# Optimization experiments

Hardware: AMD Instinct MI355X
Metric: run time of the kernel (lower is better)

Reference implementation:

```python
import jax, jax.numpy as jnp
import numpy as np

C_IN = 512
NUM_HEADS = 8
D_K = 64
D_V = 64


def setup_inputs() -> dict:
    key = jax.random.key(0)
    ks = jax.random.split(key, 6)
    scale = 1.0 / np.sqrt(C_IN)
    return {
        "x": jax.random.normal(ks[0], (8, C_IN, 32, 32), dtype=jnp.float32),
        "Wq": jax.random.normal(ks[1], (C_IN, NUM_HEADS * D_K), dtype=jnp.float32) * scale,
        "bq": jnp.zeros((NUM_HEADS * D_K,), dtype=jnp.float32),
        "Wk": jax.random.normal(ks[2], (C_IN, NUM_HEADS * D_K), dtype=jnp.float32) * scale,
        "bk": jnp.zeros((NUM_HEADS * D_K,), dtype=jnp.float32),
        "Wv": jax.random.normal(ks[3], (C_IN, NUM_HEADS * D_V), dtype=jnp.float32) * scale,
        "bv": jnp.zeros((NUM_HEADS * D_V,), dtype=jnp.float32),
        "Wo": jax.random.normal(ks[4], (NUM_HEADS * D_V, C_IN), dtype=jnp.float32) * scale,
        "bo": jnp.zeros((C_IN,), dtype=jnp.float32),
        "num_heads": NUM_HEADS,
    }


def reference(x, Wq, bq, Wk, bk, Wv, bv, Wo, bo, num_heads):
    B, C, H, W = x.shape
    S = H * W
    xs = x.reshape(B, C, S).transpose(0, 2, 1)  # [B, S, C]

    def split_heads(t):  # [B, S, nh*d] -> [B, nh, S, d]
        return t.reshape(B, S, num_heads, -1).transpose(0, 2, 1, 3)

    q = split_heads(xs @ Wq + bq)  # [B, nh, S, d_k]
    k = split_heads(xs @ Wk + bk)  # [B, nh, S, d_k]
    v = split_heads(xs @ Wv + bv)  # [B, nh, S, d_v]

    d_k = q.shape[-1]
    scores = jnp.einsum("bhqd,bhkd->bhqk", q, k) / jnp.sqrt(jnp.float32(d_k))
    probs = jax.nn.softmax(scores, axis=-1)
    attn = jnp.einsum("bhqk,bhkd->bhqd", probs, v)  # [B, nh, S, d_v]

    out = attn.transpose(0, 2, 1, 3).reshape(B, S, -1)  # [B, S, nh*d_v]
    out = out @ Wo + bo  # [B, S, C]
    out = out + xs  # residual
    return out.transpose(0, 2, 1).reshape(B, C, H, W)
```

## Files before the change

kernel.cpp:

```cpp
#include <hip/hip_runtime.h>

#define S_LEN 1024
#define CIN 512
#define NH 8
#define DH 64
#define NB 8

typedef short bf16x8 __attribute__((ext_vector_type(8)));
typedef float f32x4 __attribute__((ext_vector_type(4)));
typedef unsigned short u16x4 __attribute__((ext_vector_type(4)));

__device__ inline unsigned short f2bf(float f){
  union { float f; unsigned u; } v; v.f = f;
  unsigned r = v.u + 0x7FFFu + ((v.u >> 16) & 1u);
  return (unsigned short)(r >> 16);
}

__device__ inline unsigned cvt_pk_bf16(float a, float b){
  unsigned r;
  asm("v_cvt_pk_bf16_f32 %0, %1, %2" : "=v"(r) : "v"(a), "v"(b));
  return r;
}

__device__ inline void gload16(const void* g, void* l){
  __builtin_amdgcn_global_load_lds(
      (const __attribute__((address_space(1))) unsigned*)g,
      (__attribute__((address_space(3))) unsigned*)l, 16, 0, 0);
}

__device__ inline bf16x8 ldfrag(const unsigned short* lds, int row, int kbyte){
  return *(const bf16x8*)((const char*)lds + row*128 + (kbyte ^ ((row & 7) << 4)));
}

__global__ __launch_bounds__(256) void prep(const float* __restrict__ x,
    const float* __restrict__ Wq, const float* __restrict__ Wk,
    const float* __restrict__ Wv, const float* __restrict__ Wo,
    unsigned short* __restrict__ xs, unsigned short* __restrict__ Wqkt,
    unsigned short* __restrict__ Wvt, unsigned short* __restrict__ Wot){
  __shared__ unsigned short T[64*72];
  int bid = blockIdx.x, t = threadIdx.x;
  const float* src; unsigned short* dst; int ldS, r0, c0;
  if (bid < 1024){
    int b = bid >> 7, tt = bid & 127;
    src = x + (size_t)b*CIN*S_LEN; ldS = S_LEN;
    dst = xs + (size_t)b*S_LEN*CIN;
    r0 = (tt >> 4) * 64;
    c0 = (tt & 15) * 64;
  } else {
    int w = bid - 1024, mat = w >> 6, tt = w & 63;
    r0 = (tt >> 3) * 64; c0 = (tt & 7) * 64; ldS = 512;
    if (mat == 0){ src = Wq; dst = Wqkt; }
    else if (mat == 1){ src = Wk; dst = Wqkt + 512*512; }
    else if (mat == 2){ src = Wv; dst = Wvt; }
    else            { src = Wo; dst = Wot; }
  }
  int rl = t >> 4, cb = (t & 15) * 4;
  #pragma unroll
  for (int rr = 0; rr < 4; rr++){
    float4 f = *(const float4*)(src + (size_t)(r0 + rl + rr*16)*ldS + c0 + cb);
    int rc = rl + rr*16;
    T[(cb+0)*72 + rc] = f2bf(f.x);
    T[(cb+1)*72 + rc] = f2bf(f.y);
    T[(cb+2)*72 + rc] = f2bf(f.z);
    T[(cb+3)*72 + rc] = f2bf(f.w);
  }
  __syncthreads();
  int cl = t >> 2, rb = (t & 3) * 16;
  uint4 v0 = *(const uint4*)&T[cl*72 + rb];
  uint4 v1 = *(const uint4*)&T[cl*72 + rb + 8];
  *(uint4*)(dst + (size_t)(c0 + cl)*512 + r0 + rb) = v0;
  *(uint4*)(dst + (size_t)(c0 + cl)*512 + r0 + rb + 8) = v1;
}

__device__ inline void gemm128(const unsigned short* A, const unsigned short* B,
    unsigned short* As, unsigned short* Bs, f32x4 acc[4][4], int tid){
  int lane = tid & 63, w = tid >> 6;
  int wr = w >> 1, wc = w & 1;
  int srow = lane >> 3;
  int scol8 = ((lane & 7) ^ (lane >> 3)) << 3;
  for (int k0 = 0; k0 < 512; k0 += 64){
    __syncthreads();
    #pragma unroll
    for (int i = 0; i < 4; i++){
      int r0 = w*32 + i*8;
      gload16(A + (size_t)(r0 + srow)*512 + k0 + scol8, As + r0*64);
      gload16(B + (size_t)(r0 + srow)*512 + k0 + scol8, Bs + r0*64);
    }
    __syncthreads();
    #pragma unroll
    for (int kt = 0; kt < 2; kt++){
      bf16x8 af[4], bfv[4];
      #pragma unroll
      for (int i = 0; i < 4; i++){
        af[i]  = ldfrag(As, wr*64 + i*16 + (lane & 15), kt*64 + ((lane >> 4) << 4));
        bfv[i] = ldfrag(Bs, wc*64 + i*16 + (lane & 15), kt*64 + ((lane >> 4) << 4));
      }
      #pragma unroll
      for (int mi = 0; mi < 4; mi++)
        #pragma unroll
        for (int ni = 0; ni < 4; ni++)
          acc[mi][ni] = __builtin_amdgcn_mfma_f32_16x16x32_bf16(af[mi], bfv[ni], acc[mi][ni], 0,0,0);
    }
  }
}

__global__ __launch_bounds__(256) void qkv128(const unsigned short* __restrict__ xs,
    const unsigned short* __restrict__ Wqkt, const unsigned short* __restrict__ Wvt,
    const float* __restrict__ bq, const float* __restrict__ bk,
    const float* __restrict__ bv, unsigned short* __restrict__ q_ws,
    unsigned short* __restrict__ k_ws, unsigned short* __restrict__ vt_ws){
  __shared__ __align__(16) unsigned short As[8192], Bs[8192];
  int tid = threadIdx.x, lane = tid & 63, w = tid >> 6, wr = w >> 1, wc = w & 1;
  int bx = blockIdx.x, by = blockIdx.y, b = blockIdx.z;
  f32x4 acc[4][4];
  #pragma unroll
  for (int i = 0; i < 4; i++)
    #pragma unroll
    for (int j = 0; j < 4; j++) acc[i][j] = (f32x4){0.f,0.f,0.f,0.f};
  if (by < 8){
    int m0 = bx * 128, n0 = by * 128;
    gemm128(xs + (size_t)b*S_LEN*CIN + (size_t)m0*512, Wqkt + (size_t)n0*512, As, Bs, acc, tid);
    int jb = (n0 + wc*64) >> 6;
    int isK = jb >= 8, h = jb & 7;
    const float* bias = isK ? bk : bq;
    unsigned short* dst = (isK ? k_ws : q_ws) + ((size_t)(b*NH + h))*S_LEN*DH;
    #pragma unroll
    for (int nt = 0; nt < 4; nt++){
      int d = nt*16 + (lane & 15);
      float bb = bias[(jb & 7)*64 + d];
      #pragma unroll
      for (int mi = 0; mi < 4; mi++)
        #pragma unroll
        for (int r = 0; r < 4; r++){
          int s = m0 + wr*64 + mi*16 + (lane >> 4)*4 + r;
          dst[(size_t)s*DH + d] = f2bf(acc[mi][nt][r] + bb);
        }
    }
  } else {
    int m0 = (by - 8) * 128, n0 = bx * 128;
    gemm128(Wvt + (size_t)m0*512, xs + (size_t)b*S_LEN*CIN + (size_t)n0*512, As, Bs, acc, tid);
    #pragma unroll
    for (int mi = 0; mi < 4; mi++)
      #pragma unroll
      for (int r = 0; r < 4; r++){
        int j = m0 + wr*64 + mi*16 + (lane >> 4)*4 + r;
        int h = j >> 6, dv = j & 63;
        float bb = bv[j];
        unsigned short* dst = vt_ws + ((size_t)(b*NH + h)*DH + dv)*S_LEN;
        #pragma unroll
        for (int nt = 0; nt < 4; nt++){
          int s = n0 + wc*64 + nt*16 + (lane & 15);
          dst[s] = f2bf(acc[mi][nt][r] + bb);
        }
      }
  }
}

__global__ __launch_bounds__(512) void attn_fwd(const unsigned short* __restrict__ qw,
    const unsigned short* __restrict__ kw, const unsigned short* __restrict__ vtw,
    unsigned short* __restrict__ aw){
  __shared__ __align__(16) unsigned short Ks[2][4096], Vs[2][4096], Ps[8192];
  int tid = threadIdx.x, lane = tid & 63, wid = tid >> 6;
  int bid = blockIdx.x;
  int idx = bid >> 3;
  int qb = idx & 7;
  int bh = (bid & 7)*8 + (idx >> 3);
  int qrw = lane & 15, g = lane >> 4;
  int q0 = qb*128 + wid*16;
  const unsigned short* qrow = qw + ((size_t)bh*S_LEN + q0 + qrw)*DH;
  bf16x8 qf0 = *(const bf16x8*)(qrow + g*8);
  bf16x8 qf1 = *(const bf16x8*)(qrow + 32 + g*8);
  unsigned short* myP = Ps + wid*1024;
  f32x4 oacc[4];
  #pragma unroll
  for (int i = 0; i < 4; i++) oacc[i] = (f32x4){0.f,0.f,0.f,0.f};
  float mrun = -3e38f, lrun = 0.f;
  int srow = lane >> 3, scol8 = ((lane & 7) ^ (lane >> 3)) << 3;
  const unsigned short* kbase = kw + (size_t)bh*S_LEN*DH;
  const unsigned short* vbase = vtw + (size_t)bh*DH*S_LEN;
  const float SC = 0.125f * 1.44269504f;
  int r0 = wid*8;
  gload16(kbase + (size_t)(r0 + srow)*DH + scol8, Ks[0] + r0*64);
  gload16(vbase + (size_t)(r0 + srow)*S_LEN + scol8, Vs[0] + r0*64);
  __syncthreads();
  int cur = 0;

  for (int kv0 = 0; kv0 < S_LEN; kv0 += 64){
    if (kv0 + 64 < S_LEN){
      gload16(kbase + (size_t)(kv0 + 64 + r0 + srow)*DH + scol8, Ks[cur^1] + r0*64);
      gload16(vbase + (size_t)(r0 + srow)*S_LEN + kv0 + 64 + scol8, Vs[cur^1] + r0*64);
    }
    const unsigned short* Kc = Ks[cur];
    const unsigned short* Vc = Vs[cur];

    f32x4 st[4];
    #pragma unroll
    for (int mt = 0; mt < 4; mt++){
      f32x4 a = (f32x4){0.f,0.f,0.f,0.f};
      a = __builtin_amdgcn_mfma_f32_16x16x32_bf16(
            ldfrag(Kc, mt*16 + qrw, g << 4), qf0, a, 0,0,0);
      a = __builtin_amdgcn_mfma_f32_16x16x32_bf16(
            ldfrag(Kc, mt*16 + qrw, 64 + (g << 4)), qf1, a, 0,0,0);
      st[mt] = a;
    }
    float vmax = -3e38f;
    #pragma unroll
    for (int mt = 0; mt < 4; mt++)
      #pragma unroll
      for (int r = 0; r < 4; r++){
        st[mt][r] *= SC;
        vmax = fmaxf(vmax, st[mt][r]);
      }
    vmax = fmaxf(vmax, __shfl_xor(vmax, 16));
    vmax = fmaxf(vmax, __shfl_xor(vmax, 32));
    float mnew = fmaxf(mrun, vmax);
    float corr = __builtin_amdgcn_exp2f(mrun - mnew);
    float psum = 0.f;
    #pragma unroll
    for (int mt = 0; mt < 4; mt++){
      float p0 = __builtin_amdgcn_exp2f(st[mt][0] - mnew);
      float p1 = __builtin_amdgcn_exp2f(st[mt][1] - mnew);
      float p2 = __builtin_amdgcn_exp2f(st[mt][2] - mnew);
      float p3 = __builtin_amdgcn_exp2f(st[mt][3] - mnew);
      psum += (p0 + p1) + (p2 + p3);
      uint2 pw; pw.x = cvt_pk_bf16(p0, p1); pw.y = cvt_pk_bf16(p2, p3);
      *(uint2*)((char*)myP + qrw*128 + ((mt*32 + g*8) ^ ((qrw & 7) << 4))) = pw;
    }
    psum += __shfl_xor(psum, 16);
    psum += __shfl_xor(psum, 32);
    lrun = lrun * corr + psum;
    mrun = mnew;
    #pragma unroll
    for (int mt = 0; mt < 4; mt++) oacc[mt] *= corr;
    #pragma unroll
    for (int kt = 0; kt < 2; kt++){
      bf16x8 pf = *(const bf16x8*)((char*)myP + qrw*128 +
                    ((kt*64 + (g << 4)) ^ ((qrw & 7) << 4)));
      #pragma unroll
      for (int mt = 0; mt < 4; mt++)
        oacc[mt] = __builtin_amdgcn_mfma_f32_16x16x32_bf16(
            ldfrag(Vc, mt*16 + qrw, kt*64 + (g << 4)), pf, oacc[mt], 0,0,0);
    }
    __syncthreads();
    cur ^= 1;
  }
  float inv = 1.f / lrun;
  #pragma unroll
  for (int mt = 0; mt < 4; mt++){
    uint2 pw;
    pw.x = cvt_pk_bf16(oacc[mt][0] * inv, oacc[mt][1] * inv);
    pw.y = cvt_pk_bf16(oacc[mt][2] * inv, oacc[mt][3] * inv);
    *(uint2*)((char*)myP + qrw*128 + ((mt*32 + g*8) ^ ((qrw & 7) << 4))) = pw;
  }
  int b = bh >> 3, h = bh & 7;
  int rr = lane >> 2, cc = lane & 3;
  uint4 lo = *(const uint4*)((char*)myP + rr*128 + ((cc*32) ^ ((rr & 7) << 4)));
  uint4 hi = *(const uint4*)((char*)myP + rr*128 + (((cc*32) + 16) ^ ((rr & 7) << 4)));
  unsigned short* obase = aw + ((size_t)b*S_LEN + (q0 + rr))*512 + h*64 + cc*16;
  *(uint4*)obase = lo;
  *(uint4*)(obase + 8) = hi;
}

__global__ __launch_bounds__(256) void out128(const unsigned short* __restrict__ Wot,
    const unsigned short* __restrict__ aw, const float* __restrict__ bo,
    const float* __restrict__ x, float* __restrict__ out){
  __shared__ __align__(16) unsigned short As[8192], Bs[8192];
  int tid = threadIdx.x, lane = tid & 63, w = tid >> 6, wr = w >> 1, wc = w & 1;
  int m0 = blockIdx.x * 128, n0 = blockIdx.y * 128, b = blockIdx.z;
  f32x4 acc[4][4];
  #pragma unroll
  for (int i = 0; i < 4; i++)
    #pragma unroll
    for (int j = 0; j < 4; j++) acc[i][j] = (f32x4){0.f,0.f,0.f,0.f};
  gemm128(Wot + (size_t)m0*512, aw + (size_t)b*S_LEN*512 + (size_t)n0*512, As, Bs, acc, tid);
  #pragma unroll
  for (int mi = 0; mi < 4; mi++)
    #pragma unroll
    for (int r = 0; r < 4; r++){
      int c = m0 + wr*64 + mi*16 + (lane >> 4)*4 + r;
      float bb = bo[c];
      size_t rowb = ((size_t)b*CIN + c)*S_LEN;
      #pragma unroll
      for (int nt = 0; nt < 4; nt++){
        int s = n0 + wc*64 + nt*16 + (lane & 15);
        out[rowb + s] = acc[mi][nt][r] + bb + x[rowb + s];
      }
    }
}

extern "C" void kernel_launch(void* const* d_in, const int* in_sizes, int n_in,
                              void* d_out, int out_size, void* d_ws, size_t ws_size,
                              hipStream_t stream){
  const float* x  = (const float*)d_in[0];
  const float* Wq = (const float*)d_in[1];
  const float* bq = (const float*)d_in[2];
  const float* Wk = (const float*)d_in[3];
  const float* bk = (const float*)d_in[4];
  const float* Wv = (const float*)d_in[5];
  const float* bv = (const float*)d_in[6];
  const float* Wo = (const float*)d_in[7];
  const float* bo = (const float*)d_in[8];
  float* out = (float*)d_out;

  unsigned short* p = (unsigned short*)d_ws;
  const size_t xs_e   = (size_t)NB*S_LEN*CIN;
  const size_t qkv_e  = (size_t)NB*NH*S_LEN*DH;
  unsigned short* xs    = p;                 p += xs_e;
  unsigned short* Wqkt  = p;                 p += 1024*512;
  unsigned short* Wvt   = p;                 p += 512*512;
  unsigned short* Wot   = p;                 p += 512*512;
  unsigned short* q_ws  = p;                 p += qkv_e;
  unsigned short* k_ws  = p;                 p += qkv_e;
  unsigned short* vt_ws = p;                 p += qkv_e;
  unsigned short* aw    = p;                 p += qkv_e;

  prep<<<1280, 256, 0, stream>>>(x, Wq, Wk, Wv, Wo, xs, Wqkt, Wvt, Wot);
  qkv128<<<dim3(8, 12, NB), 256, 0, stream>>>(xs, Wqkt, Wvt, bq, bk, bv, q_ws, k_ws, vt_ws);
  attn_fwd<<<512, 512, 0, stream>>>(q_ws, k_ws, vt_ws, aw);
  out128<<<dim3(4, 8, NB), 256, 0, stream>>>(Wot, aw, bo, x, out);
}
```

Before: 156.5 us.

## Add lazy softmax rescaling, MFMA priority hints, and a 128x64 output GEMM tile

The attention loop now rescales the running max and accumulators only when some row's new max exceeds the old one by more than a threshold. This skips most per-tile exp and multiply work on the rescale path. The MFMA sections are wrapped in s_setprio to favour matrix issue across waves. The output projection uses a new 128x64 tile kernel with twice as many blocks to improve CU occupancy, at the cost of more global reloads of the weight tile. The lazy rescale lets probabilities exceed 1 by a bounded factor, which risks precision loss in bf16.

Result: faster. 151.8 us (-3.0%).

```diff
diff --git a/kernel.cpp b/kernel.cpp
--- a/kernel.cpp
+++ b/kernel.cpp
@@ -8,7 +8,7 @@
 
 typedef short bf16x8 __attribute__((ext_vector_type(8)));
 typedef float f32x4 __attribute__((ext_vector_type(4)));
-typedef unsigned short u16x4 __attribute__((ext_vector_type(4)));
+typedef float f32x2 __attribute__((ext_vector_type(2)));
 
 __device__ inline unsigned short f2bf(float f){
   union { float f; unsigned u; } v; v.f = f;
@@ -194,6 +194,7 @@
     const unsigned short* Vc = Vs[cur];
 
     f32x4 st[4];
+    __builtin_amdgcn_s_setprio(1);
     #pragma unroll
     for (int mt = 0; mt < 4; mt++){
       f32x4 a = (f32x4){0.f,0.f,0.f,0.f};
@@ -203,6 +204,7 @@
             ldfrag(Kc, mt*16 + qrw, 64 + (g << 4)), qf1, a, 0,0,0);
       st[mt] = a;
     }
+    __builtin_amdgcn_s_setprio(0);
     float vmax = -3e38f;
     #pragma unroll
     for (int mt = 0; mt < 4; mt++)
@@ -213,25 +215,29 @@
       }
     vmax = fmaxf(vmax, __shfl_xor(vmax, 16));
     vmax = fmaxf(vmax, __shfl_xor(vmax, 32));
-    float mnew = fmaxf(mrun, vmax);
-    float corr = __builtin_amdgcn_exp2f(mrun - mnew);
+    if (!__all(vmax <= mrun + 8.f)){
+      float mnew = fmaxf(mrun, vmax);
+      float corr = __builtin_amdgcn_exp2f(mrun - mnew);
+      lrun *= corr;
+      #pragma unroll
+      for (int mt = 0; mt < 4; mt++) oacc[mt] *= corr;
+      mrun = mnew;
+    }
     float psum = 0.f;
     #pragma unroll
     for (int mt = 0; mt < 4; mt++){
-      float p0 = __builtin_amdgcn_exp2f(st[mt][0] - mnew);
-      float p1 = __builtin_amdgcn_exp2f(st[mt][1] - mnew);
-      float p2 = __builtin_amdgcn_exp2f(st[mt][2] - mnew);
-      float p3 = __builtin_amdgcn_exp2f(st[mt][3] - mnew);
+      float p0 = __builtin_amdgcn_exp2f(st[mt][0] - mrun);
+      float p1 = __builtin_amdgcn_exp2f(st[mt][1] - mrun);
+      float p2 = __builtin_amdgcn_exp2f(st[mt][2] - mrun);
+      float p3 = __builtin_amdgcn_exp2f(st[mt][3] - mrun);
       psum += (p0 + p1) + (p2 + p3);
       uint2 pw; pw.x = cvt_pk_bf16(p0, p1); pw.y = cvt_pk_bf16(p2, p3);
       *(uint2*)((char*)myP + qrw*128 + ((mt*32 + g*8) ^ ((qrw & 7) << 4))) = pw;
     }
     psum += __shfl_xor(psum, 16);
     psum += __shfl_xor(psum, 32);
-    lrun = lrun * corr + psum;
-    mrun = mnew;
-    #pragma unroll
-    for (int mt = 0; mt < 4; mt++) oacc[mt] *= corr;
+    lrun += psum;
+    __builtin_amdgcn_s_setprio(1);
     #pragma unroll
     for (int kt = 0; kt < 2; kt++){
       bf16x8 pf = *(const bf16x8*)((char*)myP + qrw*128 +
@@ -241,6 +247,7 @@
         oacc[mt] = __builtin_amdgcn_mfma_f32_16x16x32_bf16(
             ldfrag(Vc, mt*16 + qrw, kt*64 + (g << 4)), pf, oacc[mt], 0,0,0);
     }
+    __builtin_amdgcn_s_setprio(0);
     __syncthreads();
     cur ^= 1;
   }
@@ -261,18 +268,50 @@
   *(uint4*)(obase + 8) = hi;
 }
 
-__global__ __launch_bounds__(256) void out128(const unsigned short* __restrict__ Wot,
+__global__ __launch_bounds__(256) void out64(const unsigned short* __restrict__ Wot,
     const unsigned short* __restrict__ aw, const float* __restrict__ bo,
     const float* __restrict__ x, float* __restrict__ out){
-  __shared__ __align__(16) unsigned short As[8192], Bs[8192];
+  __shared__ __align__(16) unsigned short As[8192], Bs[4096];
   int tid = threadIdx.x, lane = tid & 63, w = tid >> 6, wr = w >> 1, wc = w & 1;
-  int m0 = blockIdx.x * 128, n0 = blockIdx.y * 128, b = blockIdx.z;
-  f32x4 acc[4][4];
+  int m0 = blockIdx.x * 128, n0 = blockIdx.y * 64, b = blockIdx.z;
+  const unsigned short* A = Wot + (size_t)m0*512;
+  const unsigned short* B = aw + (size_t)b*S_LEN*512 + (size_t)n0*512;
+  int srow = lane >> 3;
+  int scol8 = ((lane & 7) ^ (lane >> 3)) << 3;
+  f32x4 acc[4][2];
   #pragma unroll
   for (int i = 0; i < 4; i++)
     #pragma unroll
-    for (int j = 0; j < 4; j++) acc[i][j] = (f32x4){0.f,0.f,0.f,0.f};
-  gemm128(Wot + (size_t)m0*512, aw + (size_t)b*S_LEN*512 + (size_t)n0*512, As, Bs, acc, tid);
+    for (int j = 0; j < 2; j++) acc[i][j] = (f32x4){0.f,0.f,0.f,0.f};
+  for (int k0 = 0; k0 < 512; k0 += 64){
+    __syncthreads();
+    #pragma unroll
+    for (int i = 0; i < 4; i++){
+      int r0 = w*32 + i*8;
+      gload16(A + (size_t)(r0 + srow)*512 + k0 + scol8, As + r0*64);
+    }
+    #pragma unroll
+    for (int i = 0; i < 2; i++){
+      int r0 = w*16 + i*8;
+      gload16(B + (size_t)(r0 + srow)*512 + k0 + scol8, Bs + r0*64);
+    }
+    __syncthreads();
+    #pragma unroll
+    for (int kt = 0; kt < 2; kt++){
+      bf16x8 af[4], bfv[2];
+      #pragma unroll
+      for (int i = 0; i < 4; i++)
+        af[i] = ldfrag(As, wr*64 + i*16 + (lane & 15), kt*64 + ((lane >> 4) << 4));
+      #pragma unroll
+      for (int i = 0; i < 2; i++)
+        bfv[i] = ldfrag(Bs, wc*32 + i*16 + (lane & 15), kt*64 + ((lane >> 4) << 4));
+      #pragma unroll
+      for (int mi = 0; mi < 4; mi++)
+        #pragma unroll
+        for (int ni = 0; ni < 2; ni++)
+          acc[mi][ni] = __builtin_amdgcn_mfma_f32_16x16x32_bf16(af[mi], bfv[ni], acc[mi][ni], 0,0,0);
+    }
+  }
   #pragma unroll
   for (int mi = 0; mi < 4; mi++)
     #pragma unroll
@@ -281,8 +320,8 @@
       float bb = bo[c];
       size_t rowb = ((size_t)b*CIN + c)*S_LEN;
       #pragma unroll
-      for (int nt = 0; nt < 4; nt++){
-        int s = n0 + wc*64 + nt*16 + (lane & 15);
+      for (int nt = 0; nt < 2; nt++){
+        int s = n0 + wc*32 + nt*16 + (lane & 15);
         out[rowb + s] = acc[mi][nt][r] + bb + x[rowb + s];
       }
     }
@@ -317,5 +356,5 @@
   prep<<<1280, 256, 0, stream>>>(x, Wq, Wk, Wv, Wo, xs, Wqkt, Wvt, Wot);
   qkv128<<<dim3(8, 12, NB), 256, 0, stream>>>(xs, Wqkt, Wvt, bq, bk, bv, q_ws, k_ws, vt_ws);
   attn_fwd<<<512, 512, 0, stream>>>(q_ws, k_ws, vt_ws, aw);
-  out128<<<dim3(4, 8, NB), 256, 0, stream>>>(Wot, aw, bo, x, out);
-}
+  out64<<<dim3(4, 16, NB), 256, 0, stream>>>(Wot, aw, bo, x, out);
+}
```
